# Optimization experiments

Hardware: AMD Instinct MI355X
Metric: run time of the kernel (lower is better)

Reference implementation:

```python
import jax, jax.numpy as jnp
import numpy as np

EMBED_DIM = 256
N_HEADS = 16
DK = EMBED_DIM // N_HEADS


def setup_inputs() -> dict:
    key = jax.random.key(0)
    ks = jax.random.split(key, 7)
    B, N, D = 32, 10000, EMBED_DIM
    scale = 1.0 / np.sqrt(D)
    ctx = jax.random.normal(ks[0], (B, D), dtype=jnp.float32)
    node_emb = jax.random.normal(ks[1], (B, N, D), dtype=jnp.float32)
    feas_mask = jax.random.randint(ks[2], (B, N), 0, 2).astype(jnp.bool_)
    Wq = jax.random.normal(ks[3], (D, D), dtype=jnp.float32) * scale
    Wk = jax.random.normal(ks[4], (D, D), dtype=jnp.float32) * scale
    Wv = jax.random.normal(ks[5], (D, D), dtype=jnp.float32) * scale
    Wo = jax.random.normal(ks[6], (D, D), dtype=jnp.float32) * scale
    return {"ctx": ctx, "node_emb": node_emb, "feas_mask": feas_mask,
            "Wq": Wq, "Wk": Wk, "Wv": Wv, "Wo": Wo}


def reference(ctx, node_emb, feas_mask, Wq, Wk, Wv, Wo):
    B, N, D = node_emb.shape
    H, dk = N_HEADS, DK
    # torch nn.Linear(no bias): y = x @ W.T
    q = (ctx @ Wq.T).reshape(B, H, dk)                    # [B,H,dk]
    k = (node_emb @ Wk.T).reshape(B, N, H, dk)            # [B,N,H,dk]
    v = (node_emb @ Wv.T).reshape(B, N, H, dk)            # [B,N,H,dk]
    logits = jnp.einsum('bhd,bnhd->bhn', q, k) / jnp.sqrt(jnp.float32(dk))
    neg_inf = jnp.finfo(logits.dtype).min
    logits = jnp.where(feas_mask[:, None, :], logits, neg_inf)
    attn = jax.nn.softmax(logits, axis=-1)                # [B,H,N]
    head_ctx = jnp.einsum('bhn,bnhd->bhd', attn, v)       # [B,H,dk]
    out = head_ctx.reshape(B, D)
    return out @ Wo.T
```

## Files before the change

kernel.cpp:

```cpp
#include <hip/hip_runtime.h>
#include <math.h>

#define NB 32
#define NN 10000
#define DIM 256
#define NH 16
#define NPART 16
#define PREC2 4112
#define IDXSTRIDE 10240

typedef short short8v __attribute__((ext_vector_type(8)));
typedef float float4v __attribute__((ext_vector_type(4)));

__device__ __forceinline__ unsigned bf16rne(float f) {
    unsigned u = __float_as_uint(f);
    return (u + 0x7FFFu + ((u >> 16) & 1u)) >> 16;
}
__device__ __forceinline__ unsigned pack2(float a, float b) {
    return bf16rne(a) | (bf16rne(b) << 16);
}
__device__ __forceinline__ short8v pack8(float4 A, float4 B) {
    union { short8v s; unsigned u[4]; } r;
    r.u[0] = pack2(A.x, A.y); r.u[1] = pack2(A.z, A.w);
    r.u[2] = pack2(B.x, B.y); r.u[3] = pack2(B.z, B.w);
    return r.s;
}
#define SWB(d) ((((d) >> 1) & 7) << 4)

__device__ __forceinline__ void barrier_keep_vmcnt() {
    __builtin_amdgcn_sched_barrier(0);
    asm volatile("s_waitcnt lgkmcnt(0)");
    __builtin_amdgcn_s_barrier();
    __builtin_amdgcn_sched_barrier(0);
}

__global__ void prep_compact_kernel(const float* __restrict__ ctx,
                                    const float* __restrict__ Wq,
                                    const float* __restrict__ Wk,
                                    const void* __restrict__ maskp,
                                    float* __restrict__ wt,
                                    int* __restrict__ idx,
                                    int* __restrict__ cnt) {
    int bid = blockIdx.x;
    int t = threadIdx.x, lane = t & 63, w = t >> 6;

    __shared__ float ctxL[DIM];
    __shared__ float qL[64];
    __shared__ int sflag;
    __shared__ int wcnt[4];

    if (bid < 4 * NB) {
        int b = bid >> 2, iq = bid & 3;
        ctxL[t] = ctx[b * DIM + t];
        __syncthreads();

        float4 c = ((const float4*)ctxL)[lane];
        for (int i = iq * 64 + w; i < iq * 64 + 64; i += 4) {
            float4 wq = ((const float4*)(Wq + (size_t)i * DIM))[lane];
            float s = wq.x * c.x + wq.y * c.y + wq.z * c.z + wq.w * c.w;
            #pragma unroll
            for (int off = 1; off < 64; off <<= 1) s += __shfl_xor(s, off, 64);
            if (lane == 0) qL[i - iq * 64] = s;
        }
        __syncthreads();

        #pragma unroll
        for (int hh = 0; hh < 4; ++hh) {
            int h = iq * 4 + hh;
            float a = 0.f;
            #pragma unroll
            for (int j = 0; j < 16; ++j)
                a += qL[hh * 16 + j] * Wk[(size_t)(h * 16 + j) * DIM + t];
            wt[((size_t)b * NH + h) * DIM + t] = 0.25f * a;
        }
    } else {
        int b = bid - 4 * NB;
        const int* wordbase = (const int*)maskp + (size_t)b * (NN / 4);
        int bad = 0;
        for (int i = t; i < NN / 4; i += 256)
            if ((unsigned)wordbase[i] > 1u) bad = 1;
        if (t == 0) sflag = 0;
        __syncthreads();
        if (bad) sflag = 1;
        __syncthreads();
        const bool bytemask = (sflag != 0);
        const unsigned char* m8 = (const unsigned char*)maskp + (size_t)b * NN;
        const int* m32 = (const int*)maskp + (size_t)b * NN;

        int segbeg = w * (NN / 4);
        int segend = segbeg + (NN / 4);

        int c1 = 0;
        for (int base = segbeg; base < segend; base += 64) {
            int i = base + lane;
            int pred = (i < segend) ? (bytemask ? (m8[i] != 0) : (m32[i] != 0)) : 0;
            unsigned long long bal = __ballot(pred);
            c1 += __popcll(bal);
        }
        if (lane == 0) wcnt[w] = c1;
        __syncthreads();

        int run = 0;
        for (int k = 0; k < w; ++k) run += wcnt[k];

        int* ob = idx + (size_t)b * IDXSTRIDE;
        for (int base = segbeg; base < segend; base += 64) {
            int i = base + lane;
            int pred = (i < segend) ? (bytemask ? (m8[i] != 0) : (m32[i] != 0)) : 0;
            unsigned long long bal = __ballot(pred);
            int rank = __popcll(bal & ((1ull << lane) - 1ull));
            if (pred) ob[run + rank] = i;
            run += __popcll(bal);
        }
        if (t == 0) cnt[b] = wcnt[0] + wcnt[1] + wcnt[2] + wcnt[3];
    }
}

#define XTBUF(bb) (smem + (size_t)(bb) * 32768)
#define PLBUF(bb) (smem + 65536 + (size_t)(bb) * 2304)

#define STEP_A(cc) { \
    short8v af = pack8(LA##cc, LB##cc); \
    union { short8v s; unsigned short u[8]; } U; U.s = af; \
    int d0 = g * 8 + cc * 32; \
    _Pragma("unroll") \
    for (int j = 0; j < 8; ++j) \
        *(unsigned short*)(XTc + (size_t)(d0 + j) * 128 + \
                           (ln2 ^ SWB(d0 + j))) = U.u[j]; \
    acc = __builtin_amdgcn_mfma_f32_16x16x32_bf16(af, wfrag##cc, acc, 0, 0, 0); \
}

#define PHASE_A_TAIL(tb_, cur_) { \
    char* XTc = XTBUF(cur_); char* PLc = PLBUF(cur_); \
    float4v acc = (float4v){0.f, 0.f, 0.f, 0.f}; \
    STEP_A(0) STEP_A(1) STEP_A(2) STEP_A(3) \
    STEP_A(4) STEP_A(5) STEP_A(6) STEP_A(7) \
    int mb_ = (tb_) + 16 * w + 4 * g; \
    float p0 = (mb_ + 0 < n1) ? __expf(acc[0]) : 0.f; \
    float p1 = (mb_ + 1 < n1) ? __expf(acc[1]) : 0.f; \
    float p2 = (mb_ + 2 < n1) ? __expf(acc[2]) : 0.f; \
    float p3 = (mb_ + 3 < n1) ? __expf(acc[3]) : 0.f; \
    float ts = p0 + p1 + p2 + p3; \
    ts += __shfl_xor(ts, 16, 64); \
    ts += __shfl_xor(ts, 32, 64); \
    lacc += ts; \
    *(uint2*)(PLc + hq * 144 + (16 * w + 4 * g) * 2) = \
        make_uint2(pack2(p0, p1), pack2(p2, p3)); \
}

#define PHASE_B(bb) { \
    char* XTp = XTBUF(bb); char* PLp = PLBUF(bb); \
    _Pragma("unroll") \
    for (int chunk = 0; chunk < 2; ++chunk) { \
        short8v pf = *(const short8v*)(PLp + hq * 144 + chunk * 64 + g * 16); \
        int d0 = 64 * w + hq; \
        short8v xf0 = *(const short8v*)(XTp + (size_t)(d0) * 128 + \
                                        ((chunk * 64 + g * 16) ^ SWB(d0))); \
        short8v xf1 = *(const short8v*)(XTp + (size_t)(d0 + 16) * 128 + \
                                        ((chunk * 64 + g * 16) ^ SWB(d0 + 16))); \
        short8v xf2 = *(const short8v*)(XTp + (size_t)(d0 + 32) * 128 + \
                                        ((chunk * 64 + g * 16) ^ SWB(d0 + 32))); \
        short8v xf3 = *(const short8v*)(XTp + (size_t)(d0 + 48) * 128 + \
                                        ((chunk * 64 + g * 16) ^ SWB(d0 + 48))); \
        accB0 = __builtin_amdgcn_mfma_f32_16x16x32_bf16(xf0, pf, accB0, 0, 0, 0); \
        accB1 = __builtin_amdgcn_mfma_f32_16x16x32_bf16(xf1, pf, accB1, 0, 0, 0); \
        accB2 = __builtin_amdgcn_mfma_f32_16x16x32_bf16(xf2, pf, accB2, 0, 0, 0); \
        accB3 = __builtin_amdgcn_mfma_f32_16x16x32_bf16(xf3, pf, accB3, 0, 0, 0); \
    } \
}

#define LOAD_TILE(nextpos_) { \
    const float* arow = nb + (size_t)ni * DIM + g * 8; \
    LA0 = *(const float4*)(arow + 0);   LB0 = *(const float4*)(arow + 4); \
    LA1 = *(const float4*)(arow + 32);  LB1 = *(const float4*)(arow + 36); \
    LA2 = *(const float4*)(arow + 64);  LB2 = *(const float4*)(arow + 68); \
    LA3 = *(const float4*)(arow + 96);  LB3 = *(const float4*)(arow + 100); \
    LA4 = *(const float4*)(arow + 128); LB4 = *(const float4*)(arow + 132); \
    LA5 = *(const float4*)(arow + 160); LB5 = *(const float4*)(arow + 164); \
    LA6 = *(const float4*)(arow + 192); LB6 = *(const float4*)(arow + 196); \
    LA7 = *(const float4*)(arow + 224); LB7 = *(const float4*)(arow + 228); \
    ni = ib[nextpos_]; \
    __builtin_amdgcn_sched_group_barrier(0x20, 17, 0); \
}

#define CLAMPPOS(base_) ((base_) + 16 * w + hq > cnt - 1 ? cnt - 1 : (base_) + 16 * w + hq)

__launch_bounds__(256, 2)
__global__ void attend_kernel(const float* __restrict__ node,
                              const int* __restrict__ idx,
                              const int* __restrict__ cntarr,
                              const float* __restrict__ wt,
                              float* __restrict__ partials) {
    __shared__ __align__(16) char smem[70400];
    float* LL = (float*)(smem + 70144);

    int b = blockIdx.x / NPART;
    int part = blockIdx.x % NPART;
    int t = threadIdx.x, lane = t & 63;
    int w = __builtin_amdgcn_readfirstlane(t >> 6);
    int hq = lane & 15, g = lane >> 4;

    int cnt = cntarr[b];
    int psz = ((cnt + NPART * 64 - 1) / (NPART * 64)) * 64;
    int n0 = part * psz;
    int n1 = n0 + psz; if (n1 > cnt) n1 = cnt;

    const float* nb = node + (size_t)b * NN * DIM;
    const int* ib = idx + (size_t)b * IDXSTRIDE;

    short8v wfrag0, wfrag1, wfrag2, wfrag3, wfrag4, wfrag5, wfrag6, wfrag7;
    {
        const float* wrow = wt + ((size_t)b * NH + hq) * DIM + g * 8;
        #define WLOAD(cc) wfrag##cc = pack8(*(const float4*)(wrow + cc * 32), \
                                            *(const float4*)(wrow + cc * 32 + 4));
        WLOAD(0) WLOAD(1) WLOAD(2) WLOAD(3) WLOAD(4) WLOAD(5) WLOAD(6) WLOAD(7)
        #undef WLOAD
    }

    float4v accB0 = (float4v){0.f,0.f,0.f,0.f};
    float4v accB1 = accB0, accB2 = accB0, accB3 = accB0;
    float lacc = 0.f;
    int ln2 = (16 * w + hq) * 2;

    float4 LA0, LA1, LA2, LA3, LA4, LA5, LA6, LA7;
    float4 LB0, LB1, LB2, LB3, LB4, LB5, LB6, LB7;
    int ni;

    if (n0 < n1) {
        int nt = (n1 - n0 + 63) >> 6;

        ni = ib[CLAMPPOS(n0)];
        LOAD_TILE(CLAMPPOS(n0 + 64))
        PHASE_A_TAIL(n0, 0)
        if (nt > 1) {
            LOAD_TILE(CLAMPPOS(n0 + 128))
        }
        barrier_keep_vmcnt();

        for (int tb = n0 + 64; tb < n1; tb += 64) {
            int k = (tb - n0) >> 6;
            int cur = k & 1;
            PHASE_B(cur ^ 1)
            PHASE_A_TAIL(tb, cur)
            if (tb + 64 < n1) {
                LOAD_TILE(CLAMPPOS(tb + 128))
            }
            barrier_keep_vmcnt();
        }

        PHASE_B((nt - 1) & 1)
    }

    __syncthreads();
    float* GL = (float*)smem;
    #pragma unroll
    for (int r = 0; r < 4; ++r) {
        GL[hq * 260 + 64 * w +  0 + 4 * g + r] = accB0[r];
        GL[hq * 260 + 64 * w + 16 + 4 * g + r] = accB1[r];
        GL[hq * 260 + 64 * w + 32 + 4 * g + r] = accB2[r];
        GL[hq * 260 + 64 * w + 48 + 4 * g + r] = accB3[r];
    }
    if (lane < 16) LL[w * 16 + lane] = lacc;
    __syncthreads();

    float* rec = partials + (size_t)blockIdx.x * PREC2;
    if (t < NH) rec[t] = LL[t] + LL[16 + t] + LL[32 + t] + LL[48 + t];
    for (int i = t; i < NH * DIM; i += 256)
        rec[16 + i] = GL[(i >> 8) * 260 + (i & 255)];
}

__global__ void reduce_hc_kernel(const float* __restrict__ partials,
                                 const float* __restrict__ Wv,
                                 float* __restrict__ hcws) {
    int b = blockIdx.x >> 4, h = blockIdx.x & 15;
    int t = threadIdx.x;
    __shared__ float grow[DIM];
    __shared__ float lp[NPART];
    __shared__ float lsum;

    const float* pb = partials + (size_t)b * NPART * PREC2;
    float a = 0.f;
    for (int p = 0; p < NPART; ++p) a += pb[(size_t)p * PREC2 + 16 + h * DIM + t];
    grow[t] = a;
    if (t < NPART) lp[t] = pb[(size_t)t * PREC2 + h];
    __syncthreads();
    if (t == 0) {
        float s = 0.f;
        #pragma unroll
        for (int p = 0; p < NPART; ++p) s += lp[p];
        lsum = s;
    }
    __syncthreads();

    int i = h * 16 + (t >> 4), sub = t & 15;
    const float4* wrow = (const float4*)(Wv + (size_t)i * DIM + sub * 16);
    const float4* gr = (const float4*)(grow + sub * 16);
    float s = 0.f;
    #pragma unroll
    for (int k = 0; k < 4; ++k) {
        float4 wv = wrow[k], gv = gr[k];
        s += wv.x * gv.x + wv.y * gv.y + wv.z * gv.z + wv.w * gv.w;
    }
    s += __shfl_xor(s, 1, 64);
    s += __shfl_xor(s, 2, 64);
    s += __shfl_xor(s, 4, 64);
    s += __shfl_xor(s, 8, 64);
    if (sub == 0) hcws[(size_t)b * DIM + i] = s / lsum;
}

__global__ void out_kernel(const float* __restrict__ hcws,
                           const float* __restrict__ Wo,
                           float* __restrict__ out) {
    int b = blockIdx.x >> 3, o = blockIdx.x & 7;
    int t = threadIdx.x;
    int e = o * 32 + (t >> 3), sub = t & 7;
    const float4* wrow = (const float4*)(Wo + (size_t)e * DIM + sub * 32);
    const float4* hrow = (const float4*)(hcws + (size_t)b * DIM + sub * 32);
    float a = 0.f;
    #pragma unroll
    for (int k = 0; k < 8; ++k) {
        float4 wv = wrow[k], hv = hrow[k];
        a += wv.x * hv.x + wv.y * hv.y + wv.z * hv.z + wv.w * hv.w;
    }
    a += __shfl_xor(a, 1, 64);
    a += __shfl_xor(a, 2, 64);
    a += __shfl_xor(a, 4, 64);
    if (sub == 0) out[(size_t)b * DIM + e] = a;
}

extern "C" void kernel_launch(void* const* d_in, const int* in_sizes, int n_in,
                              void* d_out, int out_size, void* d_ws, size_t ws_size,
                              hipStream_t stream) {
    const float* ctx  = (const float*)d_in[0];
    const float* node = (const float*)d_in[1];
    const void*  mask = (const void*)d_in[2];
    const float* Wq   = (const float*)d_in[3];
    const float* Wk   = (const float*)d_in[4];
    const float* Wv   = (const float*)d_in[5];
    const float* Wo   = (const float*)d_in[6];
    float* out = (float*)d_out;

    float* wsf = (float*)d_ws;
    float* wt = wsf;
    float* hcws = wt + (size_t)NB * NH * DIM;
    int*   cnt = (int*)(hcws + (size_t)NB * DIM);
    int*   idx = cnt + 256;
    float* partials = (float*)(idx + (size_t)NB * IDXSTRIDE);

    prep_compact_kernel<<<NB * 4 + NB, 256, 0, stream>>>(ctx, Wq, Wk, mask, wt, idx, cnt);
    attend_kernel<<<NB * NPART, 256, 0, stream>>>(node, idx, cnt, wt, partials);
    reduce_hc_kernel<<<NB * 16, 256, 0, stream>>>(partials, Wv, hcws);
    out_kernel<<<NB * 8, 256, 0, stream>>>(hcws, Wo, out);
}
```

Before: 70.93 us.

## Fuse all four stages into one cooperative kernel with grid syncs

Merges the prep/compact, attend, reduce and output kernels into a single cooperative mega-kernel separated by grid-wide syncs, removing three kernel launch boundaries. The host checks cooperative launch support and occupancy (512 blocks need 2 per CU), and falls back to the original four-kernel path otherwise. The trade-off is grid.sync cost, idle blocks in the small phases, and per-call host attribute and occupancy queries.

```diff
diff --git a/kernel.cpp b/kernel.cpp
--- a/kernel.cpp
+++ b/kernel.cpp
@@ -1,5 +1,8 @@
 #include <hip/hip_runtime.h>
+#include <hip/hip_cooperative_groups.h>
 #include <math.h>
+
+namespace cg = cooperative_groups;
 
 #define NB 32
 #define NN 10000
@@ -32,88 +35,6 @@
     asm volatile("s_waitcnt lgkmcnt(0)");
     __builtin_amdgcn_s_barrier();
     __builtin_amdgcn_sched_barrier(0);
-}
-
-__global__ void prep_compact_kernel(const float* __restrict__ ctx,
-                                    const float* __restrict__ Wq,
-                                    const float* __restrict__ Wk,
-                                    const void* __restrict__ maskp,
-                                    float* __restrict__ wt,
-                                    int* __restrict__ idx,
-                                    int* __restrict__ cnt) {
-    int bid = blockIdx.x;
-    int t = threadIdx.x, lane = t & 63, w = t >> 6;
-
-    __shared__ float ctxL[DIM];
-    __shared__ float qL[64];
-    __shared__ int sflag;
-    __shared__ int wcnt[4];
-
-    if (bid < 4 * NB) {
-        int b = bid >> 2, iq = bid & 3;
-        ctxL[t] = ctx[b * DIM + t];
-        __syncthreads();
-
-        float4 c = ((const float4*)ctxL)[lane];
-        for (int i = iq * 64 + w; i < iq * 64 + 64; i += 4) {
-            float4 wq = ((const float4*)(Wq + (size_t)i * DIM))[lane];
-            float s = wq.x * c.x + wq.y * c.y + wq.z * c.z + wq.w * c.w;
-            #pragma unroll
-            for (int off = 1; off < 64; off <<= 1) s += __shfl_xor(s, off, 64);
-            if (lane == 0) qL[i - iq * 64] = s;
-        }
-        __syncthreads();
-
-        #pragma unroll
-        for (int hh = 0; hh < 4; ++hh) {
-            int h = iq * 4 + hh;
-            float a = 0.f;
-            #pragma unroll
-            for (int j = 0; j < 16; ++j)
-                a += qL[hh * 16 + j] * Wk[(size_t)(h * 16 + j) * DIM + t];
-            wt[((size_t)b * NH + h) * DIM + t] = 0.25f * a;
-        }
-    } else {
-        int b = bid - 4 * NB;
-        const int* wordbase = (const int*)maskp + (size_t)b * (NN / 4);
-        int bad = 0;
-        for (int i = t; i < NN / 4; i += 256)
-            if ((unsigned)wordbase[i] > 1u) bad = 1;
-        if (t == 0) sflag = 0;
-        __syncthreads();
-        if (bad) sflag = 1;
-        __syncthreads();
-        const bool bytemask = (sflag != 0);
-        const unsigned char* m8 = (const unsigned char*)maskp + (size_t)b * NN;
-        const int* m32 = (const int*)maskp + (size_t)b * NN;
-
-        int segbeg = w * (NN / 4);
-        int segend = segbeg + (NN / 4);
-
-        int c1 = 0;
-        for (int base = segbeg; base < segend; base += 64) {
-            int i = base + lane;
-            int pred = (i < segend) ? (bytemask ? (m8[i] != 0) : (m32[i] != 0)) : 0;
-            unsigned long long bal = __ballot(pred);
-            c1 += __popcll(bal);
-        }
-        if (lane == 0) wcnt[w] = c1;
-        __syncthreads();
-
-        int run = 0;
-        for (int k = 0; k < w; ++k) run += wcnt[k];
-
-        int* ob = idx + (size_t)b * IDXSTRIDE;
-        for (int base = segbeg; base < segend; base += 64) {
-            int i = base + lane;
-            int pred = (i < segend) ? (bytemask ? (m8[i] != 0) : (m32[i] != 0)) : 0;
-            unsigned long long bal = __ballot(pred);
-            int rank = __popcll(bal & ((1ull << lane) - 1ull));
-            if (pred) ob[run + rank] = i;
-            run += __popcll(bal);
-        }
-        if (t == 0) cnt[b] = wcnt[0] + wcnt[1] + wcnt[2] + wcnt[3];
-    }
 }
 
 #define XTBUF(bb) (smem + (size_t)(bb) * 32768)
@@ -185,88 +106,248 @@
 
 #define CLAMPPOS(base_) ((base_) + 16 * w + hq > cnt - 1 ? cnt - 1 : (base_) + 16 * w + hq)
 
+#define ATTEND_BODY(bid_) { \
+    float* LL = (float*)(smem + 70144); \
+    int b = (bid_) / NPART; \
+    int part = (bid_) % NPART; \
+    int w = __builtin_amdgcn_readfirstlane(t >> 6); \
+    int hq = lane & 15, g = lane >> 4; \
+    int cnt = cntp[b]; \
+    int psz = ((cnt + NPART * 64 - 1) / (NPART * 64)) * 64; \
+    int n0 = part * psz; \
+    int n1 = n0 + psz; if (n1 > cnt) n1 = cnt; \
+    const float* nb = node + (size_t)b * NN * DIM; \
+    const int* ib = idx + (size_t)b * IDXSTRIDE; \
+    short8v wfrag0, wfrag1, wfrag2, wfrag3, wfrag4, wfrag5, wfrag6, wfrag7; \
+    { \
+        const float* wrow = wt + ((size_t)b * NH + hq) * DIM + g * 8; \
+        wfrag0 = pack8(*(const float4*)(wrow + 0),   *(const float4*)(wrow + 4)); \
+        wfrag1 = pack8(*(const float4*)(wrow + 32),  *(const float4*)(wrow + 36)); \
+        wfrag2 = pack8(*(const float4*)(wrow + 64),  *(const float4*)(wrow + 68)); \
+        wfrag3 = pack8(*(const float4*)(wrow + 96),  *(const float4*)(wrow + 100)); \
+        wfrag4 = pack8(*(const float4*)(wrow + 128), *(const float4*)(wrow + 132)); \
+        wfrag5 = pack8(*(const float4*)(wrow + 160), *(const float4*)(wrow + 164)); \
+        wfrag6 = pack8(*(const float4*)(wrow + 192), *(const float4*)(wrow + 196)); \
+        wfrag7 = pack8(*(const float4*)(wrow + 224), *(const float4*)(wrow + 228)); \
+    } \
+    float4v accB0 = (float4v){0.f,0.f,0.f,0.f}; \
+    float4v accB1 = accB0, accB2 = accB0, accB3 = accB0; \
+    float lacc = 0.f; \
+    int ln2 = (16 * w + hq) * 2; \
+    float4 LA0, LA1, LA2, LA3, LA4, LA5, LA6, LA7; \
+    float4 LB0, LB1, LB2, LB3, LB4, LB5, LB6, LB7; \
+    int ni; \
+    if (n0 < n1) { \
+        int nt = (n1 - n0 + 63) >> 6; \
+        ni = ib[CLAMPPOS(n0)]; \
+        LOAD_TILE(CLAMPPOS(n0 + 64)) \
+        PHASE_A_TAIL(n0, 0) \
+        if (nt > 1) { \
+            LOAD_TILE(CLAMPPOS(n0 + 128)) \
+        } \
+        barrier_keep_vmcnt(); \
+        for (int tb = n0 + 64; tb < n1; tb += 64) { \
+            int k = (tb - n0) >> 6; \
+            int cur = k & 1; \
+            PHASE_B(cur ^ 1) \
+            PHASE_A_TAIL(tb, cur) \
+            if (tb + 64 < n1) { \
+                LOAD_TILE(CLAMPPOS(tb + 128)) \
+            } \
+            barrier_keep_vmcnt(); \
+        } \
+        PHASE_B((nt - 1) & 1) \
+    } \
+    __syncthreads(); \
+    float* GL = (float*)smem; \
+    _Pragma("unroll") \
+    for (int r = 0; r < 4; ++r) { \
+        GL[hq * 260 + 64 * w +  0 + 4 * g + r] = accB0[r]; \
+        GL[hq * 260 + 64 * w + 16 + 4 * g + r] = accB1[r]; \
+        GL[hq * 260 + 64 * w + 32 + 4 * g + r] = accB2[r]; \
+        GL[hq * 260 + 64 * w + 48 + 4 * g + r] = accB3[r]; \
+    } \
+    if (lane < 16) LL[w * 16 + lane] = lacc; \
+    __syncthreads(); \
+    float* rec = partials + (size_t)(bid_) * PREC2; \
+    if (t < NH) rec[t] = LL[t] + LL[16 + t] + LL[32 + t] + LL[48 + t]; \
+    for (int i = t; i < NH * DIM; i += 256) \
+        rec[16 + i] = GL[(i >> 8) * 260 + (i & 255)]; \
+}
+
+#define PREP_BODY(bid_) { \
+    int w = t >> 6; \
+    int b = (bid_) >> 2, iq = (bid_) & 3; \
+    float* ctxL = (float*)smem; \
+    float* qL = (float*)(smem + 1024); \
+    ctxL[t] = ctx[b * DIM + t]; \
+    __syncthreads(); \
+    float4 c = ((const float4*)ctxL)[lane]; \
+    for (int i = iq * 64 + w; i < iq * 64 + 64; i += 4) { \
+        float4 wq = ((const float4*)(Wq + (size_t)i * DIM))[lane]; \
+        float s = wq.x * c.x + wq.y * c.y + wq.z * c.z + wq.w * c.w; \
+        _Pragma("unroll") \
+        for (int off = 1; off < 64; off <<= 1) s += __shfl_xor(s, off, 64); \
+        if (lane == 0) qL[i - iq * 64] = s; \
+    } \
+    __syncthreads(); \
+    _Pragma("unroll") \
+    for (int hh = 0; hh < 4; ++hh) { \
+        int h = iq * 4 + hh; \
+        float a = 0.f; \
+        _Pragma("unroll") \
+        for (int j = 0; j < 16; ++j) \
+            a += qL[hh * 16 + j] * Wk[(size_t)(h * 16 + j) * DIM + t]; \
+        wt[((size_t)b * NH + h) * DIM + t] = 0.25f * a; \
+    } \
+}
+
+#define COMPACT_BODY(b_) { \
+    int w = t >> 6; \
+    int b = (b_); \
+    int* sflag = (int*)smem; \
+    int* wcnt = (int*)(smem + 16); \
+    const int* wordbase = (const int*)maskp + (size_t)b * (NN / 4); \
+    int bad = 0; \
+    for (int i = t; i < NN / 4; i += 256) \
+        if ((unsigned)wordbase[i] > 1u) bad = 1; \
+    if (t == 0) *sflag = 0; \
+    __syncthreads(); \
+    if (bad) *sflag = 1; \
+    __syncthreads(); \
+    const bool bytemask = (*sflag != 0); \
+    const unsigned char* m8 = (const unsigned char*)maskp + (size_t)b * NN; \
+    const int* m32 = (const int*)maskp + (size_t)b * NN; \
+    int segbeg = w * (NN / 4); \
+    int segend = segbeg + (NN / 4); \
+    int c1 = 0; \
+    for (int base = segbeg; base < segend; base += 64) { \
+        int i = base + lane; \
+        int pred = (i < segend) ? (bytemask ? (m8[i] != 0) : (m32[i] != 0)) : 0; \
+        unsigned long long bal = __ballot(pred); \
+        c1 += __popcll(bal); \
+    } \
+    if (lane == 0) wcnt[w] = c1; \
+    __syncthreads(); \
+    int run = 0; \
+    for (int k = 0; k < w; ++k) run += wcnt[k]; \
+    int* ob = idx + (size_t)b * IDXSTRIDE; \
+    for (int base = segbeg; base < segend; base += 64) { \
+        int i = base + lane; \
+        int pred = (i < segend) ? (bytemask ? (m8[i] != 0) : (m32[i] != 0)) : 0; \
+        unsigned long long bal = __ballot(pred); \
+        int rank = __popcll(bal & ((1ull << lane) - 1ull)); \
+        if (pred) ob[run + rank] = i; \
+        run += __popcll(bal); \
+    } \
+    if (t == 0) cntp[b] = wcnt[0] + wcnt[1] + wcnt[2] + wcnt[3]; \
+}
+
+__global__ void __launch_bounds__(256, 2)
+mega_kernel(const float* __restrict__ ctx, const float* __restrict__ node,
+            const void* __restrict__ maskp,
+            const float* __restrict__ Wq, const float* __restrict__ Wk,
+            const float* __restrict__ Wv, const float* __restrict__ Wo,
+            float* __restrict__ wt, int* __restrict__ idx,
+            int* __restrict__ cntp, float* __restrict__ partials,
+            float* __restrict__ hcws, float* __restrict__ out) {
+    __shared__ __align__(16) char smem[70400];
+    cg::grid_group grid = cg::this_grid();
+    int bid = blockIdx.x;
+    int t = threadIdx.x, lane = t & 63;
+
+    if (bid < 4 * NB) {
+        PREP_BODY(bid)
+    } else if (bid < 5 * NB) {
+        COMPACT_BODY(bid - 4 * NB)
+    }
+    __threadfence();
+    grid.sync();
+
+    ATTEND_BODY(bid)
+    __threadfence();
+    grid.sync();
+
+    {
+        int b = bid >> 4, h = bid & 15;
+        float* grow = (float*)smem;
+        float* lp = (float*)(smem + 1024);
+        float* lsum = (float*)(smem + 1088);
+        const float* pb = partials + (size_t)b * NPART * PREC2;
+        float a = 0.f;
+        for (int p = 0; p < NPART; ++p) a += pb[(size_t)p * PREC2 + 16 + h * DIM + t];
+        grow[t] = a;
+        if (t < NPART) lp[t] = pb[(size_t)t * PREC2 + h];
+        __syncthreads();
+        if (t == 0) {
+            float s = 0.f;
+            #pragma unroll
+            for (int p = 0; p < NPART; ++p) s += lp[p];
+            *lsum = s;
+        }
+        __syncthreads();
+        int i = h * 16 + (t >> 4), sub = t & 15;
+        const float4* wrow = (const float4*)(Wv + (size_t)i * DIM + sub * 16);
+        const float4* gr = (const float4*)(grow + sub * 16);
+        float s = 0.f;
+        #pragma unroll
+        for (int k = 0; k < 4; ++k) {
+            float4 wv = wrow[k], gv = gr[k];
+            s += wv.x * gv.x + wv.y * gv.y + wv.z * gv.z + wv.w * gv.w;
+        }
+        s += __shfl_xor(s, 1, 64);
+        s += __shfl_xor(s, 2, 64);
+        s += __shfl_xor(s, 4, 64);
+        s += __shfl_xor(s, 8, 64);
+        if (sub == 0) hcws[(size_t)b * DIM + i] = s / *lsum;
+    }
+    __threadfence();
+    grid.sync();
+
+    if (bid < NB * 8) {
+        int b = bid >> 3, o = bid & 7;
+        int e = o * 32 + (t >> 3), sub = t & 7;
+        const float4* wrow = (const float4*)(Wo + (size_t)e * DIM + sub * 32);
+        const float4* hrow = (const float4*)(hcws + (size_t)b * DIM + sub * 32);
+        float a = 0.f;
+        #pragma unroll
+        for (int k = 0; k < 8; ++k) {
+            float4 wv = wrow[k], hv = hrow[k];
+            a += wv.x * hv.x + wv.y * hv.y + wv.z * hv.z + wv.w * hv.w;
+        }
+        a += __shfl_xor(a, 1, 64);
+        a += __shfl_xor(a, 2, 64);
+        a += __shfl_xor(a, 4, 64);
+        if (sub == 0) out[(size_t)b * DIM + e] = a;
+    }
+}
+
+__global__ void prep_compact_kernel(const float* __restrict__ ctx,
+                                    const float* __restrict__ Wq,
+                                    const float* __restrict__ Wk,
+                                    const void* __restrict__ maskp,
+                                    float* __restrict__ wt,
+                                    int* __restrict__ idx,
+                                    int* __restrict__ cntp) {
+    __shared__ __align__(16) char smem[1312];
+    int bid = blockIdx.x;
+    int t = threadIdx.x, lane = t & 63;
+    if (bid < 4 * NB) {
+        PREP_BODY(bid)
+    } else {
+        COMPACT_BODY(bid - 4 * NB)
+    }
+}
+
 __launch_bounds__(256, 2)
 __global__ void attend_kernel(const float* __restrict__ node,
                               const int* __restrict__ idx,
-                              const int* __restrict__ cntarr,
+                              const int* __restrict__ cntp,
                               const float* __restrict__ wt,
                               float* __restrict__ partials) {
     __shared__ __align__(16) char smem[70400];
-    float* LL = (float*)(smem + 70144);
-
-    int b = blockIdx.x / NPART;
-    int part = blockIdx.x % NPART;
     int t = threadIdx.x, lane = t & 63;
-    int w = __builtin_amdgcn_readfirstlane(t >> 6);
-    int hq = lane & 15, g = lane >> 4;
-
-    int cnt = cntarr[b];
-    int psz = ((cnt + NPART * 64 - 1) / (NPART * 64)) * 64;
-    int n0 = part * psz;
-    int n1 = n0 + psz; if (n1 > cnt) n1 = cnt;
-
-    const float* nb = node + (size_t)b * NN * DIM;
-    const int* ib = idx + (size_t)b * IDXSTRIDE;
-
-    short8v wfrag0, wfrag1, wfrag2, wfrag3, wfrag4, wfrag5, wfrag6, wfrag7;
-    {
-        const float* wrow = wt + ((size_t)b * NH + hq) * DIM + g * 8;
-        #define WLOAD(cc) wfrag##cc = pack8(*(const float4*)(wrow + cc * 32), \
-                                            *(const float4*)(wrow + cc * 32 + 4));
-        WLOAD(0) WLOAD(1) WLOAD(2) WLOAD(3) WLOAD(4) WLOAD(5) WLOAD(6) WLOAD(7)
-        #undef WLOAD
-    }
-
-    float4v accB0 = (float4v){0.f,0.f,0.f,0.f};
-    float4v accB1 = accB0, accB2 = accB0, accB3 = accB0;
-    float lacc = 0.f;
-    int ln2 = (16 * w + hq) * 2;
-
-    float4 LA0, LA1, LA2, LA3, LA4, LA5, LA6, LA7;
-    float4 LB0, LB1, LB2, LB3, LB4, LB5, LB6, LB7;
-    int ni;
-
-    if (n0 < n1) {
-        int nt = (n1 - n0 + 63) >> 6;
-
-        ni = ib[CLAMPPOS(n0)];
-        LOAD_TILE(CLAMPPOS(n0 + 64))
-        PHASE_A_TAIL(n0, 0)
-        if (nt > 1) {
-            LOAD_TILE(CLAMPPOS(n0 + 128))
-        }
-        barrier_keep_vmcnt();
-
-        for (int tb = n0 + 64; tb < n1; tb += 64) {
-            int k = (tb - n0) >> 6;
-            int cur = k & 1;
-            PHASE_B(cur ^ 1)
-            PHASE_A_TAIL(tb, cur)
-            if (tb + 64 < n1) {
-                LOAD_TILE(CLAMPPOS(tb + 128))
-            }
-            barrier_keep_vmcnt();
-        }
-
-        PHASE_B((nt - 1) & 1)
-    }
-
-    __syncthreads();
-    float* GL = (float*)smem;
-    #pragma unroll
-    for (int r = 0; r < 4; ++r) {
-        GL[hq * 260 + 64 * w +  0 + 4 * g + r] = accB0[r];
-        GL[hq * 260 + 64 * w + 16 + 4 * g + r] = accB1[r];
-        GL[hq * 260 + 64 * w + 32 + 4 * g + r] = accB2[r];
-        GL[hq * 260 + 64 * w + 48 + 4 * g + r] = accB3[r];
-    }
-    if (lane < 16) LL[w * 16 + lane] = lacc;
-    __syncthreads();
-
-    float* rec = partials + (size_t)blockIdx.x * PREC2;
-    if (t < NH) rec[t] = LL[t] + LL[16 + t] + LL[32 + t] + LL[48 + t];
-    for (int i = t; i < NH * DIM; i += 256)
-        rec[16 + i] = GL[(i >> 8) * 260 + (i & 255)];
+    ATTEND_BODY(blockIdx.x)
 }
 
 __global__ void reduce_hc_kernel(const float* __restrict__ partials,
@@ -277,7 +358,6 @@
     __shared__ float grow[DIM];
     __shared__ float lp[NPART];
     __shared__ float lsum;
-
     const float* pb = partials + (size_t)b * NPART * PREC2;
     float a = 0.f;
     for (int p = 0; p < NPART; ++p) a += pb[(size_t)p * PREC2 + 16 + h * DIM + t];
@@ -291,7 +371,6 @@
         lsum = s;
     }
     __syncthreads();
-
     int i = h * 16 + (t >> 4), sub = t & 15;
     const float4* wrow = (const float4*)(Wv + (size_t)i * DIM + sub * 16);
     const float4* gr = (const float4*)(grow + sub * 16);
@@ -347,6 +426,24 @@
     int*   idx = cnt + 256;
     float* partials = (float*)(idx + (size_t)NB * IDXSTRIDE);
 
+    int dev = 0;
+    hipGetDevice(&dev);
+    int coopAttr = 0, ncu = 0, nb = 0;
+    hipDeviceGetAttribute(&coopAttr, hipDeviceAttributeCooperativeLaunch, dev);
+    hipDeviceGetAttribute(&ncu, hipDeviceAttributeMultiprocessorCount, dev);
+    hipOccupancyMaxActiveBlocksPerMultiprocessor(&nb, (const void*)mega_kernel, 256, 0);
+
+    if (coopAttr && (long)nb * ncu >= NB * NPART) {
+        void* args[] = { (void*)&ctx, (void*)&node, (void*)&mask,
+                         (void*)&Wq, (void*)&Wk, (void*)&Wv, (void*)&Wo,
+                         (void*)&wt, (void*)&idx, (void*)&cnt,
+                         (void*)&partials, (void*)&hcws, (void*)&out };
+        hipError_t e = hipLaunchCooperativeKernel((const void*)mega_kernel,
+                                                  dim3(NB * NPART), dim3(256),
+                                                  args, 0, stream);
+        if (e == hipSuccess) return;
+    }
+
     prep_compact_kernel<<<NB * 4 + NB, 256, 0, stream>>>(ctx, Wq, Wk, mask, wt, idx, cnt);
     attend_kernel<<<NB * NPART, 256, 0, stream>>>(node, idx, cnt, wt, partials);
     reduce_hc_kernel<<<NB * 16, 256, 0, stream>>>(partials, Wv, hcws);
```

Result: no change. 70.82 us (-0.2%).

## Single-buffer LDS tiles to fit three blocks per CU and raise partitions

Applied to the files above, without the earlier changes.

Drops the double-buffered LDS staging (XT/PL buffers) to a single buffer, halving shared memory to about 35KB so launch bounds can request 3 blocks per CU. A second barrier is added between phase B and phase A each iteration to protect the single buffer. The number of N partitions per batch rises from 16 to 24 to put more blocks in the grid. The extra barrier serializes the two phases within a block, which is traded for more concurrent blocks and a tighter register budget.

```diff
diff --git a/kernel.cpp b/kernel.cpp
--- a/kernel.cpp
+++ b/kernel.cpp
@@ -5,7 +5,7 @@
 #define NN 10000
 #define DIM 256
 #define NH 16
-#define NPART 16
+#define NPART 24
 #define PREC2 4112
 #define IDXSTRIDE 10240
 
@@ -33,91 +33,6 @@
     __builtin_amdgcn_s_barrier();
     __builtin_amdgcn_sched_barrier(0);
 }
-
-__global__ void prep_compact_kernel(const float* __restrict__ ctx,
-                                    const float* __restrict__ Wq,
-                                    const float* __restrict__ Wk,
-                                    const void* __restrict__ maskp,
-                                    float* __restrict__ wt,
-                                    int* __restrict__ idx,
-                                    int* __restrict__ cnt) {
-    int bid = blockIdx.x;
-    int t = threadIdx.x, lane = t & 63, w = t >> 6;
-
-    __shared__ float ctxL[DIM];
-    __shared__ float qL[64];
-    __shared__ int sflag;
-    __shared__ int wcnt[4];
-
-    if (bid < 4 * NB) {
-        int b = bid >> 2, iq = bid & 3;
-        ctxL[t] = ctx[b * DIM + t];
-        __syncthreads();
-
-        float4 c = ((const float4*)ctxL)[lane];
-        for (int i = iq * 64 + w; i < iq * 64 + 64; i += 4) {
-            float4 wq = ((const float4*)(Wq + (size_t)i * DIM))[lane];
-            float s = wq.x * c.x + wq.y * c.y + wq.z * c.z + wq.w * c.w;
-            #pragma unroll
-            for (int off = 1; off < 64; off <<= 1) s += __shfl_xor(s, off, 64);
-            if (lane == 0) qL[i - iq * 64] = s;
-        }
-        __syncthreads();
-
-        #pragma unroll
-        for (int hh = 0; hh < 4; ++hh) {
-            int h = iq * 4 + hh;
-            float a = 0.f;
-            #pragma unroll
-            for (int j = 0; j < 16; ++j)
-                a += qL[hh * 16 + j] * Wk[(size_t)(h * 16 + j) * DIM + t];
-            wt[((size_t)b * NH + h) * DIM + t] = 0.25f * a;
-        }
-    } else {
-        int b = bid - 4 * NB;
-        const int* wordbase = (const int*)maskp + (size_t)b * (NN / 4);
-        int bad = 0;
-        for (int i = t; i < NN / 4; i += 256)
-            if ((unsigned)wordbase[i] > 1u) bad = 1;
-        if (t == 0) sflag = 0;
-        __syncthreads();
-        if (bad) sflag = 1;
-        __syncthreads();
-        const bool bytemask = (sflag != 0);
-        const unsigned char* m8 = (const unsigned char*)maskp + (size_t)b * NN;
-        const int* m32 = (const int*)maskp + (size_t)b * NN;
-
-        int segbeg = w * (NN / 4);
-        int segend = segbeg + (NN / 4);
-
-        int c1 = 0;
-        for (int base = segbeg; base < segend; base += 64) {
-            int i = base + lane;
-            int pred = (i < segend) ? (bytemask ? (m8[i] != 0) : (m32[i] != 0)) : 0;
-            unsigned long long bal = __ballot(pred);
-            c1 += __popcll(bal);
-        }
-        if (lane == 0) wcnt[w] = c1;
-        __syncthreads();
-
-        int run = 0;
-        for (int k = 0; k < w; ++k) run += wcnt[k];
-
-        int* ob = idx + (size_t)b * IDXSTRIDE;
-        for (int base = segbeg; base < segend; base += 64) {
-            int i = base + lane;
-            int pred = (i < segend) ? (bytemask ? (m8[i] != 0) : (m32[i] != 0)) : 0;
-            unsigned long long bal = __ballot(pred);
-            int rank = __popcll(bal & ((1ull << lane) - 1ull));
-            if (pred) ob[run + rank] = i;
-            run += __popcll(bal);
-        }
-        if (t == 0) cnt[b] = wcnt[0] + wcnt[1] + wcnt[2] + wcnt[3];
-    }
-}
-
-#define XTBUF(bb) (smem + (size_t)(bb) * 32768)
-#define PLBUF(bb) (smem + 65536 + (size_t)(bb) * 2304)
 
 #define STEP_A(cc) { \
     short8v af = pack8(LA##cc, LB##cc); \
@@ -125,13 +40,12 @@
     int d0 = g * 8 + cc * 32; \
     _Pragma("unroll") \
     for (int j = 0; j < 8; ++j) \
-        *(unsigned short*)(XTc + (size_t)(d0 + j) * 128 + \
+        *(unsigned short*)(smem + (size_t)(d0 + j) * 128 + \
                            (ln2 ^ SWB(d0 + j))) = U.u[j]; \
     acc = __builtin_amdgcn_mfma_f32_16x16x32_bf16(af, wfrag##cc, acc, 0, 0, 0); \
 }
 
-#define PHASE_A_TAIL(tb_, cur_) { \
-    char* XTc = XTBUF(cur_); char* PLc = PLBUF(cur_); \
+#define PHASE_A_TAIL(tb_) { \
     float4v acc = (float4v){0.f, 0.f, 0.f, 0.f}; \
     STEP_A(0) STEP_A(1) STEP_A(2) STEP_A(3) \
     STEP_A(4) STEP_A(5) STEP_A(6) STEP_A(7) \
@@ -144,23 +58,22 @@
     ts += __shfl_xor(ts, 16, 64); \
     ts += __shfl_xor(ts, 32, 64); \
     lacc += ts; \
-    *(uint2*)(PLc + hq * 144 + (16 * w + 4 * g) * 2) = \
+    *(uint2*)(smem + 32768 + hq * 144 + (16 * w + 4 * g) * 2) = \
         make_uint2(pack2(p0, p1), pack2(p2, p3)); \
 }
 
-#define PHASE_B(bb) { \
-    char* XTp = XTBUF(bb); char* PLp = PLBUF(bb); \
+#define PHASE_B() { \
     _Pragma("unroll") \
     for (int chunk = 0; chunk < 2; ++chunk) { \
-        short8v pf = *(const short8v*)(PLp + hq * 144 + chunk * 64 + g * 16); \
+        short8v pf = *(const short8v*)(smem + 32768 + hq * 144 + chunk * 64 + g * 16); \
         int d0 = 64 * w + hq; \
-        short8v xf0 = *(const short8v*)(XTp + (size_t)(d0) * 128 + \
+        short8v xf0 = *(const short8v*)(smem + (size_t)(d0) * 128 + \
                                         ((chunk * 64 + g * 16) ^ SWB(d0))); \
-        short8v xf1 = *(const short8v*)(XTp + (size_t)(d0 + 16) * 128 + \
+        short8v xf1 = *(const short8v*)(smem + (size_t)(d0 + 16) * 128 + \
                                         ((chunk * 64 + g * 16) ^ SWB(d0 + 16))); \
-        short8v xf2 = *(const short8v*)(XTp + (size_t)(d0 + 32) * 128 + \
+        short8v xf2 = *(const short8v*)(smem + (size_t)(d0 + 32) * 128 + \
                                         ((chunk * 64 + g * 16) ^ SWB(d0 + 32))); \
-        short8v xf3 = *(const short8v*)(XTp + (size_t)(d0 + 48) * 128 + \
+        short8v xf3 = *(const short8v*)(smem + (size_t)(d0 + 48) * 128 + \
                                         ((chunk * 64 + g * 16) ^ SWB(d0 + 48))); \
         accB0 = __builtin_amdgcn_mfma_f32_16x16x32_bf16(xf0, pf, accB0, 0, 0, 0); \
         accB1 = __builtin_amdgcn_mfma_f32_16x16x32_bf16(xf1, pf, accB1, 0, 0, 0); \
@@ -185,22 +98,104 @@
 
 #define CLAMPPOS(base_) ((base_) + 16 * w + hq > cnt - 1 ? cnt - 1 : (base_) + 16 * w + hq)
 
-__launch_bounds__(256, 2)
+__global__ void prep_compact_kernel(const float* __restrict__ ctx,
+                                    const float* __restrict__ Wq,
+                                    const float* __restrict__ Wk,
+                                    const void* __restrict__ maskp,
+                                    float* __restrict__ wt,
+                                    int* __restrict__ idx,
+                                    int* __restrict__ cntp) {
+    int bid = blockIdx.x;
+    int t = threadIdx.x, lane = t & 63, w = t >> 6;
+
+    __shared__ float ctxL[DIM];
+    __shared__ float qL[64];
+    __shared__ int sflag;
+    __shared__ int wcnt[4];
+
+    if (bid < 4 * NB) {
+        int b = bid >> 2, iq = bid & 3;
+        ctxL[t] = ctx[b * DIM + t];
+        __syncthreads();
+
+        float4 c = ((const float4*)ctxL)[lane];
+        for (int i = iq * 64 + w; i < iq * 64 + 64; i += 4) {
+            float4 wq = ((const float4*)(Wq + (size_t)i * DIM))[lane];
+            float s = wq.x * c.x + wq.y * c.y + wq.z * c.z + wq.w * c.w;
+            #pragma unroll
+            for (int off = 1; off < 64; off <<= 1) s += __shfl_xor(s, off, 64);
+            if (lane == 0) qL[i - iq * 64] = s;
+        }
+        __syncthreads();
+
+        #pragma unroll
+        for (int hh = 0; hh < 4; ++hh) {
+            int h = iq * 4 + hh;
+            float a = 0.f;
+            #pragma unroll
+            for (int j = 0; j < 16; ++j)
+                a += qL[hh * 16 + j] * Wk[(size_t)(h * 16 + j) * DIM + t];
+            wt[((size_t)b * NH + h) * DIM + t] = 0.25f * a;
+        }
+    } else {
+        int b = bid - 4 * NB;
+        const int* wordbase = (const int*)maskp + (size_t)b * (NN / 4);
+        int bad = 0;
+        for (int i = t; i < NN / 4; i += 256)
+            if ((unsigned)wordbase[i] > 1u) bad = 1;
+        if (t == 0) sflag = 0;
+        __syncthreads();
+        if (bad) sflag = 1;
+        __syncthreads();
+        const bool bytemask = (sflag != 0);
+        const unsigned char* m8 = (const unsigned char*)maskp + (size_t)b * NN;
+        const int* m32 = (const int*)maskp + (size_t)b * NN;
+
+        int segbeg = w * (NN / 4);
+        int segend = segbeg + (NN / 4);
+
+        int c1 = 0;
+        for (int base = segbeg; base < segend; base += 64) {
+            int i = base + lane;
+            int pred = (i < segend) ? (bytemask ? (m8[i] != 0) : (m32[i] != 0)) : 0;
+            unsigned long long bal = __ballot(pred);
+            c1 += __popcll(bal);
+        }
+        if (lane == 0) wcnt[w] = c1;
+        __syncthreads();
+
+        int run = 0;
+        for (int k = 0; k < w; ++k) run += wcnt[k];
+
+        int* ob = idx + (size_t)b * IDXSTRIDE;
+        for (int base = segbeg; base < segend; base += 64) {
+            int i = base + lane;
+            int pred = (i < segend) ? (bytemask ? (m8[i] != 0) : (m32[i] != 0)) : 0;
+            unsigned long long bal = __ballot(pred);
+            int rank = __popcll(bal & ((1ull << lane) - 1ull));
+            if (pred) ob[run + rank] = i;
+            run += __popcll(bal);
+        }
+        if (t == 0) cntp[b] = wcnt[0] + wcnt[1] + wcnt[2] + wcnt[3];
+    }
+}
+
+__launch_bounds__(256, 3)
 __global__ void attend_kernel(const float* __restrict__ node,
                               const int* __restrict__ idx,
-                              const int* __restrict__ cntarr,
+                              const int* __restrict__ cntp,
                               const float* __restrict__ wt,
                               float* __restrict__ partials) {
-    __shared__ __align__(16) char smem[70400];
-    float* LL = (float*)(smem + 70144);
+    __shared__ __align__(16) char smem[35328];
+    int t = threadIdx.x, lane = t & 63;
+    float* LL = (float*)(smem + 35072);
 
     int b = blockIdx.x / NPART;
     int part = blockIdx.x % NPART;
-    int t = threadIdx.x, lane = t & 63;
     int w = __builtin_amdgcn_readfirstlane(t >> 6);
     int hq = lane & 15, g = lane >> 4;
 
-    int cnt = cntarr[b];
+    int cnt = cntp[b];
     int psz = ((cnt + NPART * 64 - 1) / (NPART * 64)) * 64;
     int n0 = part * psz;
     int n1 = n0 + psz; if (n1 > cnt) n1 = cnt;
@@ -211,10 +206,14 @@
     short8v wfrag0, wfrag1, wfrag2, wfrag3, wfrag4, wfrag5, wfrag6, wfrag7;
     {
         const float* wrow = wt + ((size_t)b * NH + hq) * DIM + g * 8;
-        #define WLOAD(cc) wfrag##cc = pack8(*(const float4*)(wrow + cc * 32), \
-                                            *(const float4*)(wrow + cc * 32 + 4));
-        WLOAD(0) WLOAD(1) WLOAD(2) WLOAD(3) WLOAD(4) WLOAD(5) WLOAD(6) WLOAD(7)
-        #undef WLOAD
+        wfrag0 = pack8(*(const float4*)(wrow + 0),   *(const float4*)(wrow + 4));
+        wfrag1 = pack8(*(const float4*)(wrow + 32),  *(const float4*)(wrow + 36));
+        wfrag2 = pack8(*(const float4*)(wrow + 64),  *(const float4*)(wrow + 68));
+        wfrag3 = pack8(*(const float4*)(wrow + 96),  *(const float4*)(wrow + 100));
+        wfrag4 = pack8(*(const float4*)(wrow + 128), *(const float4*)(wrow + 132));
+        wfrag5 = pack8(*(const float4*)(wrow + 160), *(const float4*)(wrow + 164));
+        wfrag6 = pack8(*(const float4*)(wrow + 192), *(const float4*)(wrow + 196));
+        wfrag7 = pack8(*(const float4*)(wrow + 224), *(const float4*)(wrow + 228));
     }
 
     float4v accB0 = (float4v){0.f,0.f,0.f,0.f};
@@ -227,28 +226,25 @@
     int ni;
 
     if (n0 < n1) {
-        int nt = (n1 - n0 + 63) >> 6;
-
         ni = ib[CLAMPPOS(n0)];
         LOAD_TILE(CLAMPPOS(n0 + 64))
-        PHASE_A_TAIL(n0, 0)
-        if (nt > 1) {
+        PHASE_A_TAIL(n0)
+        if (n0 + 64 < n1) {
             LOAD_TILE(CLAMPPOS(n0 + 128))
         }
         barrier_keep_vmcnt();
 
         for (int tb = n0 + 64; tb < n1; tb += 64) {
-            int k = (tb - n0) >> 6;
-            int cur = k & 1;
-            PHASE_B(cur ^ 1)
-            PHASE_A_TAIL(tb, cur)
+            PHASE_B()
+            barrier_keep_vmcnt();
+            PHASE_A_TAIL(tb)
             if (tb + 64 < n1) {
                 LOAD_TILE(CLAMPPOS(tb + 128))
             }
             barrier_keep_vmcnt();
         }
 
-        PHASE_B((nt - 1) & 1)
+        PHASE_B()
     }
 
     __syncthreads();
```

Measured after the change: 115.2 us. 1.62x slower.
